# Optimization experiments

Measured on AMD Instinct MI355X. Metric: run time of the kernel, lower is better.

The kernel has to match this reference:

```python
import jax, jax.numpy as jnp
import numpy as np

H = 8            # n_heads
CAP = 512        # capacity
TOPK = 2
N_HOPS = 2
ROPE_BASE = 10000.0
VOCAB = 32000
D = 512


def rope_cos_sin(T, dh, base):
    inv = 1.0 / (base ** (jnp.arange(0, dh, 2, dtype=jnp.float32) / dh))
    f = jnp.arange(T, dtype=jnp.float32)[:, None] * inv[None, :]   # [T, dh/2]
    emb = jnp.concatenate([f, f], axis=-1)                          # [T, dh]
    return jnp.cos(emb), jnp.sin(emb)


def rmsnorm(x, s):
    return x * jax.lax.rsqrt(jnp.mean(x * x, axis=-1, keepdims=True) + 1e-6) * s


def rotate_half(x):
    x1, x2 = jnp.split(x, 2, axis=-1)
    return jnp.concatenate([-x2, x1], axis=-1)


def attn_block(x, cos, sin, wqkv, wo, ln_s):
    # pre-norm causal attention with RoPE; residual included (module returns x + attn)
    C, d = x.shape
    dh = d // H
    u = rmsnorm(x, ln_s)
    qkv = u @ wqkv.T                                   # [C, 3d]
    q, k, v = [t.reshape(C, H, dh) for t in jnp.split(qkv, 3, axis=-1)]
    c = cos[:, None, :]; s = sin[:, None, :]
    q = q * c + rotate_half(q) * s
    k = k * c + rotate_half(k) * s
    scores = jnp.einsum('qhd,khd->hqk', q, k) / jnp.sqrt(jnp.float32(dh))
    causal = jnp.tril(jnp.ones((C, C), dtype=bool))
    scores = jnp.where(causal[None], scores, -1e9)
    a = jax.nn.softmax(scores, axis=-1)
    o = jnp.einsum('hqk,khd->qhd', a, v).reshape(C, d)
    return x + o @ wo.T


def ffn_block(x, w1, w2, ln_s):
    u = rmsnorm(x, ln_s)
    return x + jax.nn.gelu(u @ w1.T) @ w2.T


def hop(h, wr, attn_qkv, attn_o, attn_ln, ffn_w1, ffn_w2, ffn_ln, cos, sin):
    T, d = h.shape
    E_total = wr.shape[0]
    E = E_total - 1                                    # last expert = identity
    logits = h @ wr.T                                  # [T, E_total]
    probs = jax.nn.softmax(logits, axis=-1)
    _, idx = jax.lax.top_k(logits, TOPK)
    mask = jax.nn.one_hot(idx, E_total).sum(axis=-2) > 0     # [T, E_total]
    probs_tr = probs[:, :-1]
    mask_tr = mask[:, :-1]
    # capacity select: per-expert top-cap gated tokens -> one-hot slot [E, cap, T]
    g = jnp.where(mask_tr.T, probs_tr.T, -jnp.inf)     # [E, T]
    cap = min(CAP, T)
    _, top_idx = jax.lax.top_k(g, cap)                 # [E, cap]
    slot = jnp.zeros((E, cap, T), jnp.float32).at[
        jnp.arange(E)[:, None], jnp.arange(cap)[None, :], top_idx].set(1.0)
    slot = slot * mask_tr.T[:, None, :]
    kept = slot.sum(axis=1) > 0                        # [E, T]
    # dispatch
    xin = jnp.einsum('ect,td->ecd', slot, h)
    cos_r = jnp.einsum('ect,td->ecd', slot, cos)
    sin_r = jnp.einsum('ect,td->ecd', slot, sin)
    attn_idx = jnp.arange(0, E, 2)
    ffn_idx = jnp.arange(1, E, 2)
    out_a = jax.vmap(attn_block)(xin[attn_idx], cos_r[attn_idx], sin_r[attn_idx],
                                 attn_qkv, attn_o, attn_ln)
    out_f = jax.vmap(ffn_block)(xin[ffn_idx], ffn_w1, ffn_w2, ffn_ln)
    expert_out = jnp.zeros_like(xin).at[attn_idx].set(out_a).at[ffn_idx].set(out_f)
    # combine
    combine_w = jnp.where(kept.T, probs_tr, 0.0)       # [T, E]
    rho = combine_w.sum(axis=-1, keepdims=True)        # [T, 1]
    combine = jnp.einsum('ecd,ect,et->td', expert_out, slot, combine_w.T)
    return h + combine - rho * h


def setup_inputs() -> dict:
    key = jax.random.key(0)
    ks = jax.random.split(key, 12)
    T = 2048
    sc = 0.02
    return {
        'ids': jax.random.randint(ks[0], (T,), 0, VOCAB),
        'embed_w': jax.random.normal(ks[1], (VOCAB, D), jnp.float32) * sc,
        'router_w': jax.random.normal(ks[2], (N_HOPS, 9, D), jnp.float32) * sc,
        'attn_qkv': jax.random.normal(ks[3], (4, 3 * D, D), jnp.float32) * sc,
        'attn_o': jax.random.normal(ks[4], (4, D, D), jnp.float32) * sc,
        'attn_ln': jnp.ones((4, D), jnp.float32),
        'ffn_w1': jax.random.normal(ks[5], (4, 4 * D, D), jnp.float32) * sc,
        'ffn_w2': jax.random.normal(ks[6], (4, D, 4 * D), jnp.float32) * sc,
        'ffn_ln': jnp.ones((4, D), jnp.float32),
        'bb_qkv': jax.random.normal(ks[7], (3 * D, D), jnp.float32) * sc,
        'bb_o': jax.random.normal(ks[8], (D, D), jnp.float32) * sc,
        'bb_ln': jnp.ones((D,), jnp.float32),
        'lnout_s': jnp.ones((D,), jnp.float32),
    }


def reference(ids, embed_w, router_w, attn_qkv, attn_o, attn_ln,
              ffn_w1, ffn_w2, ffn_ln, bb_qkv, bb_o, bb_ln, lnout_s):
    T = ids.shape[0]
    dh = D // H
    h = embed_w[ids]                                   # [T, D]
    cos, sin = rope_cos_sin(T, dh, ROPE_BASE)
    h = attn_block(h, cos, sin, bb_qkv, bb_o, bb_ln)   # backbone (num_backbone=1)
    for i in range(router_w.shape[0]):                 # n_hops routed layers
        h = hop(h, router_w[i], attn_qkv, attn_o, attn_ln,
                ffn_w1, ffn_w2, ffn_ln, cos, sin)
    return rmsnorm(h, lnout_s)
```

## Files before the change

### kernel.cpp

```cpp
#include <hip/hip_runtime.h>
#include <hip/hip_bf16.h>

#define T_SEQ 2048
#define DMODEL 512
#define CEXP 512

typedef short s16x4 __attribute__((ext_vector_type(4)));
typedef short s16x8 __attribute__((ext_vector_type(8)));
typedef float f32x4 __attribute__((ext_vector_type(4)));

__device__ __forceinline__ float geluf(float x){
  float x3 = x*x*x;
  return 0.5f*x*(1.f + tanhf(0.7978845608028654f*(x + 0.044715f*x3)));
}

__device__ __forceinline__ unsigned short f2b(float x){
  unsigned int u = __float_as_uint(x);
  u += 0x7fffu + ((u >> 16) & 1u);
  return (unsigned short)(u >> 16);
}

struct GP {
  const float* A; long As;
  const float* W; long Ws;
  const float* R; long Rs;
  float* O; long Os;
  int M, N, K, act;
};

__global__ void embed_kernel(const int* __restrict__ ids, const float* __restrict__ ew,
                             float* __restrict__ h){
  int idx = blockIdx.x*256 + threadIdx.x;
  int t = idx >> 9, d = idx & 511;
  h[idx] = ew[(size_t)ids[t]*DMODEL + d];
}

__global__ void rope_table_kernel(float* __restrict__ cosb, float* __restrict__ sinb){
  int idx = blockIdx.x*256 + threadIdx.x;
  int t = idx >> 6, i = idx & 63, j = i & 31;
  float inv = powf(10000.f, -(float)(2*j)/64.f);
  float a = (float)t * inv;
  cosb[idx] = cosf(a);
  sinb[idx] = sinf(a);
}

__global__ void rmsnorm_kernel(const float* __restrict__ in, float* __restrict__ out,
                               const float* __restrict__ scale,
                               int rows_per_group, long gstride, int scale_stride){
  int row = blockIdx.x;
  int g = row / rows_per_group, lr = row - g*rows_per_group;
  const float* x = in  + (size_t)g*gstride + (size_t)lr*DMODEL;
  float*       y = out + (size_t)g*gstride + (size_t)lr*DMODEL;
  const float* s = scale + (size_t)g*scale_stride;
  int tid = threadIdx.x;
  float ss = 0.f;
  for (int i = tid; i < DMODEL; i += 256){ float v = x[i]; ss += v*v; }
  __shared__ float red[256];
  red[tid] = ss; __syncthreads();
  for (int st = 128; st > 0; st >>= 1){ if (tid < st) red[tid] += red[tid+st]; __syncthreads(); }
  float r = rsqrtf(red[0]*(1.f/DMODEL) + 1e-6f);
  for (int i = tid; i < DMODEL; i += 256) y[i] = x[i]*r*s[i];
}

__global__ void final_rmsnorm_kernel(const float* __restrict__ in, float* __restrict__ out,
                                     const float* __restrict__ scale){
  int row = blockIdx.x;
  const float* x = in + (size_t)row*DMODEL;
  int tid = threadIdx.x;
  float ss = 0.f;
  for (int i = tid; i < DMODEL; i += 256){ float v = x[i]; ss += v*v; }
  __shared__ float red[256];
  red[tid] = ss; __syncthreads();
  for (int st = 128; st > 0; st >>= 1){ if (tid < st) red[tid] += red[tid+st]; __syncthreads(); }
  float r = rsqrtf(red[0]*(1.f/DMODEL) + 1e-6f);
  for (int i = tid; i < DMODEL; i += 256)
    out[(size_t)row*DMODEL + i] = x[i]*r*scale[i];
}

__device__ __forceinline__ void gemm64_body(GP g, int bx, int by, int bz){
  const float* A = g.A + (size_t)bz*g.As;
  const float* W = g.W + (size_t)bz*g.Ws;
  const float* Res = g.R ? g.R + (size_t)bz*g.Rs : nullptr;
  float* Out = g.O + (size_t)bz*g.Os;
  int M = g.M, N = g.N, K = g.K, act = g.act;
  __shared__ float As[16][68];
  __shared__ float Ws[16][68];
  int tid = threadIdx.x;
  int tx = tid & 15, ty = tid >> 4;
  int row0 = bx*64, col0 = by*64;
  float acc[4][4] = {{0.f}};
  int sm = tid >> 2;
  int skq = (tid & 3) << 2;
  int gm = row0 + sm, gn = col0 + sm;

  float4 va = make_float4(0.f,0.f,0.f,0.f);
  float4 vw = make_float4(0.f,0.f,0.f,0.f);
  if (gm < M) va = *(const float4*)&A[(size_t)gm*K + skq];
  if (gn < N) vw = *(const float4*)&W[(size_t)gn*K + skq];

  for (int k0 = 0; k0 < K; k0 += 16){
    __syncthreads();
    As[skq+0][sm] = va.x; As[skq+1][sm] = va.y; As[skq+2][sm] = va.z; As[skq+3][sm] = va.w;
    Ws[skq+0][sm] = vw.x; Ws[skq+1][sm] = vw.y; Ws[skq+2][sm] = vw.z; Ws[skq+3][sm] = vw.w;
    __syncthreads();
    if (k0 + 16 < K){
      if (gm < M) va = *(const float4*)&A[(size_t)gm*K + k0 + 16 + skq];
      if (gn < N) vw = *(const float4*)&W[(size_t)gn*K + k0 + 16 + skq];
    }
    #pragma unroll
    for (int kk = 0; kk < 16; ++kk){
      float4 av = *(const float4*)&As[kk][ty*4];
      float4 wv = *(const float4*)&Ws[kk][tx*4];
      float a[4] = {av.x, av.y, av.z, av.w};
      float w[4] = {wv.x, wv.y, wv.z, wv.w};
      #pragma unroll
      for (int i = 0; i < 4; ++i)
        #pragma unroll
        for (int j = 0; j < 4; ++j)
          acc[i][j] += a[i]*w[j];
    }
  }
  #pragma unroll
  for (int i = 0; i < 4; ++i){
    int om = row0 + ty*4 + i;
    if (om >= M) continue;
    #pragma unroll
    for (int j = 0; j < 4; ++j){
      int on = col0 + tx*4 + j;
      if (on >= N) continue;
      float v = acc[i][j];
      if (act == 1) v = geluf(v);
      if (Res) v += Res[(size_t)om*N + on];
      Out[(size_t)om*N + on] = v;
    }
  }
}

__global__ __launch_bounds__(256)
void gemm_kernel(GP g){ gemm64_body(g, blockIdx.x, blockIdx.y, blockIdx.z); }

__global__ __launch_bounds__(256)
void gemm_dual(GP g1, GP g2, int ysplit){
  bool first = (int)blockIdx.y < ysplit;
  GP g = first ? g1 : g2;
  int by = first ? blockIdx.y : blockIdx.y - ysplit;
  gemm64_body(g, blockIdx.x, by, blockIdx.z);
}

__global__ __launch_bounds__(256)
void gemm128(const float* __restrict__ A, long Astride,
             const float* __restrict__ W, long Wstride,
             const float* __restrict__ Res, long Rstride,
             float* __restrict__ Out, long Ostride,
             int M, int N, int K, int act){
  int b = blockIdx.z;
  A += (size_t)b*Astride; W += (size_t)b*Wstride; Out += (size_t)b*Ostride;
  if (Res) Res += (size_t)b*Rstride;
  __shared__ float As[16][132];
  __shared__ float Ws[16][132];
  int tid = threadIdx.x;
  int r0 = (tid >> 4) * 8;
  int c0 = (tid & 15) * 8;
  int row0 = blockIdx.x*128, col0 = blockIdx.y*128;
  int sr = tid >> 1;
  int sc = (tid & 1) * 8;
  float acc[8][8] = {{0.f}};

  float4 a0 = *(const float4*)&A[(size_t)(row0+sr)*K + sc];
  float4 a1 = *(const float4*)&A[(size_t)(row0+sr)*K + sc + 4];
  float4 w0 = *(const float4*)&W[(size_t)(col0+sr)*K + sc];
  float4 w1 = *(const float4*)&W[(size_t)(col0+sr)*K + sc + 4];

  for (int k0 = 0; k0 < K; k0 += 16){
    __syncthreads();
    As[sc+0][sr]=a0.x; As[sc+1][sr]=a0.y; As[sc+2][sr]=a0.z; As[sc+3][sr]=a0.w;
    As[sc+4][sr]=a1.x; As[sc+5][sr]=a1.y; As[sc+6][sr]=a1.z; As[sc+7][sr]=a1.w;
    Ws[sc+0][sr]=w0.x; Ws[sc+1][sr]=w0.y; Ws[sc+2][sr]=w0.z; Ws[sc+3][sr]=w0.w;
    Ws[sc+4][sr]=w1.x; Ws[sc+5][sr]=w1.y; Ws[sc+6][sr]=w1.z; Ws[sc+7][sr]=w1.w;
    __syncthreads();
    if (k0 + 16 < K){
      a0 = *(const float4*)&A[(size_t)(row0+sr)*K + k0 + 16 + sc];
      a1 = *(const float4*)&A[(size_t)(row0+sr)*K + k0 + 16 + sc + 4];
      w0 = *(const float4*)&W[(size_t)(col0+sr)*K + k0 + 16 + sc];
      w1 = *(const float4*)&W[(size_t)(col0+sr)*K + k0 + 16 + sc + 4];
    }
    #pragma unroll
    for (int kk = 0; kk < 16; ++kk){
      float a[8], w[8];
      *(float4*)&a[0] = *(const float4*)&As[kk][r0];
      *(float4*)&a[4] = *(const float4*)&As[kk][r0+4];
      *(float4*)&w[0] = *(const float4*)&Ws[kk][c0];
      *(float4*)&w[4] = *(const float4*)&Ws[kk][c0+4];
      #pragma unroll
      for (int i = 0; i < 8; ++i)
        #pragma unroll
        for (int j = 0; j < 8; ++j)
          acc[i][j] += a[i]*w[j];
    }
  }

  #pragma unroll
  for (int i = 0; i < 8; ++i){
    int gm = row0 + r0 + i;
    #pragma unroll
    for (int jj = 0; jj < 2; ++jj){
      int gn = col0 + c0 + jj*4;
      float4 v;
      v.x = acc[i][jj*4+0]; v.y = acc[i][jj*4+1];
      v.z = acc[i][jj*4+2]; v.w = acc[i][jj*4+3];
      if (act == 1){ v.x = geluf(v.x); v.y = geluf(v.y); v.z = geluf(v.z); v.w = geluf(v.w); }
      if (Res){
        float4 rv = *(const float4*)&Res[(size_t)gm*N + gn];
        v.x += rv.x; v.y += rv.y; v.z += rv.z; v.w += rv.w;
      }
      *(float4*)&Out[(size_t)gm*N + gn] = v;
    }
  }
}

__device__ __forceinline__ void mfma_body(GP g, int bx, int by, int bz){
  const float* A = g.A + (size_t)bz*g.As;
  const float* W = g.W + (size_t)bz*g.Ws;
  const float* Res = g.R ? g.R + (size_t)bz*g.Rs : nullptr;
  float* Out = g.O + (size_t)bz*g.Os;
  int N = g.N, K = g.K, act = g.act;

  __shared__ short As[128][40];
  __shared__ short Ws[128][40];

  int tid = threadIdx.x;
  int l = tid & 63, w = tid >> 6;
  int wrow = (w >> 1)*64, wcol = (w & 1)*64;
  int row0 = bx*128, col0 = by*128;
  int lm = l & 15, lq = l >> 4;

  f32x4 acc[4][4];
  #pragma unroll
  for (int i = 0; i < 4; ++i)
    #pragma unroll
    for (int j = 0; j < 4; ++j)
      acc[i][j] = (f32x4){0.f,0.f,0.f,0.f};

  for (int k0 = 0; k0 < K; k0 += 32){
    #pragma unroll
    for (int t = 0; t < 4; ++t){
      int f4 = tid + t*256;
      int r = f4 >> 3, kq = f4 & 7;
      float4 va = *(const float4*)&A[(size_t)(row0 + r)*K + k0 + kq*4];
      s16x4 pa; pa[0]=(short)f2b(va.x); pa[1]=(short)f2b(va.y); pa[2]=(short)f2b(va.z); pa[3]=(short)f2b(va.w);
      *(s16x4*)&As[r][kq*4] = pa;
      float4 vw = *(const float4*)&W[(size_t)(col0 + r)*K + k0 + kq*4];
      s16x4 pw; pw[0]=(short)f2b(vw.x); pw[1]=(short)f2b(vw.y); pw[2]=(short)f2b(vw.z); pw[3]=(short)f2b(vw.w);
      *(s16x4*)&Ws[r][kq*4] = pw;
    }
    __syncthreads();

    s16x8 af[4], bf[4];
    #pragma unroll
    for (int rt = 0; rt < 4; ++rt)
      af[rt] = *(s16x8*)&As[wrow + rt*16 + lm][lq*8];
    #pragma unroll
    for (int ct = 0; ct < 4; ++ct)
      bf[ct] = *(s16x8*)&Ws[wcol + ct*16 + lm][lq*8];
    #pragma unroll
    for (int rt = 0; rt < 4; ++rt)
      #pragma unroll
      for (int ct = 0; ct < 4; ++ct)
        acc[rt][ct] = __builtin_amdgcn_mfma_f32_16x16x32_bf16(af[rt], bf[ct], acc[rt][ct], 0, 0, 0);
    __syncthreads();
  }

  #pragma unroll
  for (int rt = 0; rt < 4; ++rt){
    #pragma unroll
    for (int p = 0; p < 4; ++p){
      int row = row0 + wrow + rt*16 + lq*4 + p;
      #pragma unroll
      for (int ct = 0; ct < 4; ++ct){
        int col = col0 + wcol + ct*16 + lm;
        float v = acc[rt][ct][p];
        if (act == 1) v = geluf(v);
        if (Res) v += Res[(size_t)row*N + col];
        Out[(size_t)row*N + col] = v;
      }
    }
  }
}

__global__ __launch_bounds__(256)
void gemm_mfma(GP g){ mfma_body(g, blockIdx.x, blockIdx.y, blockIdx.z); }

__global__ __launch_bounds__(256)
void mfma_dual(GP g1, GP g2, int ysplit){
  bool first = (int)blockIdx.y < ysplit;
  GP g = first ? g1 : g2;
  int by = first ? blockIdx.y : blockIdx.y - ysplit;
  mfma_body(g, blockIdx.x, by, blockIdx.z);
}

__global__ void rope_kernel(float* __restrict__ qkv, const float* __restrict__ cosb,
                            const float* __restrict__ sinb, const int* __restrict__ map,
                            int map_gstride, int rows_per_group){
  int idx = blockIdx.x*256 + threadIdx.x;
  int row = idx >> 9;
  int rem = idx & 511;
  int sec = rem >> 8;
  int hh  = (rem >> 5) & 7;
  int j   = rem & 31;
  int t;
  if (map){
    t = map[(row/rows_per_group)*map_gstride + (row % rows_per_group)];
    if (t < 0) return;
  } else {
    t = row;
  }
  float c = cosb[t*64 + j], s = sinb[t*64 + j];
  float* p = qkv + (size_t)row*1536 + sec*512 + hh*64;
  float a = p[j], b = p[j+32];
  p[j]    = a*c - b*s;
  p[j+32] = b*c + a*s;
}

__global__ __launch_bounds__(256, 3)
void fattn_kernel(const float* __restrict__ qkv, float* __restrict__ ctx, int C){
  int tps = C >> 4;
  int pairs = tps >> 1;
  int lin = blockIdx.y * gridDim.x + blockIdx.x;
  int hh  = lin & 7;
  int bx  = lin >> 3;
  int seq = bx / pairs;
  int pr  = bx - seq*pairs;
  size_t base = (size_t)seq * C * 1536;
  const float* Qg = qkv + base + hh*64;
  const float* Kg = qkv + base + 512 + hh*64;
  const float* Vg = qkv + base + 1024 + hh*64;

  __shared__ float Qs[16][68];
  __shared__ float Ks[64][68];
  __shared__ float Ps[16][68];

  int tid = threadIdx.x;
  int tx = tid & 15, ty = tid >> 4;

  #pragma unroll 1
  for (int half = 0; half < 2; ++half){
    int lt = half ? pr : (tps - 1 - pr);
    int q0 = lt << 4;
    if (half) __syncthreads();

    *(float4*)&Qs[ty][tx*4] = *(const float4*)&Qg[(size_t)(q0 + ty)*1536 + tx*4];

    float o[4] = {0.f, 0.f, 0.f, 0.f};
    float mrow = -1e30f, lrow = 0.f;

    int nkt = (lt >> 2) + 1;
    for (int kt = 0; kt < nkt; ++kt){
      int k0 = kt << 6;
      if (kt) __syncthreads();
      for (int i = tid; i < 64*16; i += 256){
        int r = i >> 4, dq = i & 15;
        *(float4*)&Ks[r][dq*4] = *(const float4*)&Kg[(size_t)(k0 + r)*1536 + dq*4];
      }
      __syncthreads();

      const float* vbase = Vg + (size_t)k0*1536 + tx*4;
      float4 nv0 = *(const float4*)(vbase + 0*1536);
      float4 nv1 = *(const float4*)(vbase + 1*1536);
      float4 nv2 = *(const float4*)(vbase + 2*1536);
      float4 nv3 = *(const float4*)(vbase + 3*1536);

      float s[4] = {0.f, 0.f, 0.f, 0.f};
      #pragma unroll
      for (int d = 0; d < 64; d += 4){
        float4 qv = *(const float4*)&Qs[ty][d];
        float4 kv[4];
        #pragma unroll
        for (int j = 0; j < 4; ++j) kv[j] = *(const float4*)&Ks[j*16+tx][d];
        #pragma unroll
        for (int j = 0; j < 4; ++j)
          s[j] += qv.x*kv[j].x + qv.y*kv[j].y + qv.z*kv[j].z + qv.w*kv[j].w;
      }
      {
        int q = q0 + ty;
        #pragma unroll
        for (int j = 0; j < 4; ++j){
          int k = k0 + j*16 + tx;
          s[j] = (k <= q) ? s[j]*0.125f : -1e30f;
        }
      }
      {
        float m2 = fmaxf(fmaxf(s[0], s[1]), fmaxf(s[2], s[3]));
        #pragma unroll
        for (int off = 1; off < 16; off <<= 1)
          m2 = fmaxf(m2, __shfl_xor(m2, off, 64));
        float mnew = fmaxf(mrow, m2);
        float alpha = __expf(mrow - mnew);
        float p0 = __expf(s[0] - mnew);
        float p1 = __expf(s[1] - mnew);
        float p2 = __expf(s[2] - mnew);
        float p3 = __expf(s[3] - mnew);
        float rs = (p0 + p1) + (p2 + p3);
        #pragma unroll
        for (int off = 1; off < 16; off <<= 1)
          rs += __shfl_xor(rs, off, 64);
        lrow = lrow*alpha + rs;
        mrow = mnew;
        #pragma unroll
        for (int j = 0; j < 4; ++j) o[j] *= alpha;
        Ps[ty][tx]    = p0;
        Ps[ty][16+tx] = p1;
        Ps[ty][32+tx] = p2;
        Ps[ty][48+tx] = p3;
      }
      {
        #pragma unroll
        for (int kc = 0; kc < 16; ++kc){
          float4 v0 = nv0, v1 = nv1, v2 = nv2, v3 = nv3;
          if (kc < 15){
            const float* nb = vbase + (size_t)(kc+1)*4*1536;
            nv0 = *(const float4*)(nb + 0*1536);
            nv1 = *(const float4*)(nb + 1*1536);
            nv2 = *(const float4*)(nb + 2*1536);
            nv3 = *(const float4*)(nb + 3*1536);
          }
          float4 pr4 = *(const float4*)&Ps[ty][kc*4];
          o[0] += pr4.x*v0.x + pr4.y*v1.x + pr4.z*v2.x + pr4.w*v3.x;
          o[1] += pr4.x*v0.y + pr4.y*v1.y + pr4.z*v2.y + pr4.w*v3.y;
          o[2] += pr4.x*v0.z + pr4.y*v1.z + pr4.z*v2.z + pr4.w*v3.z;
          o[3] += pr4.x*v0.w + pr4.y*v1.w + pr4.z*v2.w + pr4.w*v3.w;
        }
      }
    }

    float inv = 1.f / lrow;
    float4 res;
    res.x = o[0]*inv; res.y = o[1]*inv; res.z = o[2]*inv; res.w = o[3]*inv;
    *(float4*)(ctx + (size_t)(seq*C + q0 + ty)*512 + hh*64 + tx*4) = res;
  }
}

__global__ void router_kernel(const float* __restrict__ logits, float* __restrict__ probs,
                              int* __restrict__ maskb){
  int t = blockIdx.x*256 + threadIdx.x;
  if (t >= T_SEQ) return;
  float v[9];
  float mx = -1e30f;
  for (int e = 0; e < 9; ++e){ v[e] = logits[t*9+e]; mx = fmaxf(mx, v[e]); }
  float s = 0.f;
  for (int e = 0; e < 9; ++e) s += expf(v[e]-mx);
  float inv = 1.f/s;
  for (int e = 0; e < 8; ++e) probs[t*8+e] = expf(v[e]-mx)*inv;
  int i1 = 0;
  for (int e = 1; e < 9; ++e) if (v[e] > v[i1]) i1 = e;
  int i2 = -1;
  for (int e = 0; e < 9; ++e){ if (e == i1) continue; if (i2 < 0 || v[e] > v[i2]) i2 = e; }
  maskb[t] = (1<<i1) | (1<<i2);
}

__global__ void seti_kernel(int* __restrict__ p, int v, int n){
  int i = blockIdx.x*256 + threadIdx.x;
  if (i < n) p[i] = v;
}

__global__ void rank_kernel(const float* __restrict__ probs, const int* __restrict__ maskb,
                            int* __restrict__ t2s, int* __restrict__ s2t, float* __restrict__ cw){
  int idx = blockIdx.x*256 + threadIdx.x;
  int e = idx / T_SEQ, t = idx - e*T_SEQ;
  __shared__ float spm[T_SEQ];
  int tid = threadIdx.x;
  for (int i = tid; i < T_SEQ; i += 256)
    spm[i] = ((maskb[i]>>e)&1) ? probs[i*8+e] : -1.0f;
  __syncthreads();
  int slot = -1; float w = 0.f;
  if ((maskb[t]>>e)&1){
    float p = probs[t*8+e];
    int rank = 0;
    #pragma unroll 8
    for (int t2 = 0; t2 < T_SEQ; ++t2){
      float p2 = spm[t2];
      rank += (p2 > p || (p2 == p && t2 < t)) ? 1 : 0;
    }
    if (rank < CEXP){ slot = rank; w = p; s2t[e*CEXP + rank] = t; }
  }
  t2s[t*8+e] = slot;
  cw[t*8+e] = w;
}

__global__ void gather_kernel(const float* __restrict__ h, const int* __restrict__ s2t,
                              float* __restrict__ xin){
  int idx = blockIdx.x*256 + threadIdx.x;
  int row = idx >> 9, d = idx & 511;
  int t = s2t[row];
  xin[idx] = (t >= 0) ? h[(size_t)t*DMODEL + d] : 0.f;
}

__global__ void combine_kernel(float* __restrict__ h, const float* __restrict__ eout,
                               const int* __restrict__ t2s, const float* __restrict__ cw){
  int idx = blockIdx.x*256 + threadIdx.x;
  int t = idx >> 9, d = idx & 511;
  float acc = 0.f, rho = 0.f;
  for (int e = 0; e < 8; ++e){
    int c = t2s[t*8+e];
    if (c >= 0){
      float w = cw[t*8+e];
      rho += w;
      acc += w * eout[((size_t)e*CEXP + c)*DMODEL + d];
    }
  }
  float hv = h[idx];
  h[idx] = hv + acc - rho*hv;
}

extern "C" void kernel_launch(void* const* d_in, const int* in_sizes, int n_in,
                              void* d_out, int out_size, void* d_ws, size_t ws_size,
                              hipStream_t stream){
  const int*   ids      = (const int*)  d_in[0];
  const float* embed_w  = (const float*)d_in[1];
  const float* router_w = (const float*)d_in[2];
  const float* attn_qkv = (const float*)d_in[3];
  const float* attn_o   = (const float*)d_in[4];
  const float* attn_ln  = (const float*)d_in[5];
  const float* ffn_w1   = (const float*)d_in[6];
  const float* ffn_w2   = (const float*)d_in[7];
  const float* ffn_ln   = (const float*)d_in[8];
  const float* bb_qkv   = (const float*)d_in[9];
  const float* bb_o     = (const float*)d_in[10];
  const float* bb_ln    = (const float*)d_in[11];
  const float* lnout_s  = (const float*)d_in[12];
  float* out = (float*)d_out;

  float* W    = (float*)d_ws;
  float* h    = W;
  float* cosb = h    + 1048576;
  float* sinb = cosb + 131072;
  float* xin  = sinb + 131072;
  float* u    = xin  + 2097152;
  float* big  = u    + 2097152;
  float* ctx  = big  + 4194304;
  float* eout = ctx  + 1048576;
  float* logits = eout + 2097152;
  float* probs  = logits + 18432;
  float* cw     = probs  + 16384;
  int* ibase = (int*)(cw + 16384);
  int* maskb = ibase;
  int* t2s   = maskb + 2048;
  int* s2t   = t2s   + 16384;

  embed_kernel<<<4096, 256, 0, stream>>>(ids, embed_w, h);
  rope_table_kernel<<<512, 256, 0, stream>>>(cosb, sinb);

  rmsnorm_kernel<<<2048, 256, 0, stream>>>(h, u, bb_ln, 2048, 0, 0);
  gemm128<<<dim3(16,12,1), 256, 0, stream>>>(u, 0, bb_qkv, 0, nullptr, 0, big, 0,
                                             2048, 1536, 512, 0);
  rope_kernel<<<4096, 256, 0, stream>>>(big, cosb, sinb, nullptr, 0, 2048);
  fattn_kernel<<<dim3(64,8,1), 256, 0, stream>>>(big, ctx, 2048);
  gemm_kernel<<<dim3(32,8,1), 256, 0, stream>>>(
      GP{ctx, 0, bb_o, 0, h, 0, h, 0, 2048, 512, 512, 0});

  for (int hop = 0; hop < 2; ++hop){
    const float* wr = router_w + (size_t)hop*9*512;
    gemm_kernel<<<dim3(32,1,1), 256, 0, stream>>>(
        GP{h, 0, wr, 0, nullptr, 0, logits, 0, 2048, 9, 512, 0});
    router_kernel<<<8, 256, 0, stream>>>(logits, probs, maskb);
    seti_kernel<<<16, 256, 0, stream>>>(s2t, -1, 4096);
    rank_kernel<<<64, 256, 0, stream>>>(probs, maskb, t2s, s2t, cw);
    gather_kernel<<<8192, 256, 0, stream>>>(h, s2t, xin);

    rmsnorm_kernel<<<2048, 256, 0, stream>>>(xin,          u,          attn_ln, 512, 524288, 512);
    rmsnorm_kernel<<<2048, 256, 0, stream>>>(xin + 262144, u + 262144, ffn_ln,  512, 524288, 512);

    if (hop == 0){
      gemm128<<<dim3(4,12,4), 256, 0, stream>>>(u, 524288, attn_qkv, 786432, nullptr, 0,
                                                big, 786432, 512, 1536, 512, 0);
      rope_kernel<<<4096, 256, 0, stream>>>(big, cosb, sinb, s2t, 1024, 512);
      fattn_kernel<<<dim3(64,8,1), 256, 0, stream>>>(big, ctx, 512);
      gemm128<<<dim3(4,16,4), 256, 0, stream>>>(u + 262144, 524288, ffn_w1, 1048576,
                                                nullptr, 0, big, 1048576,
                                                512, 2048, 512, 1);
      gemm_dual<<<dim3(8,16,4), 256, 0, stream>>>(
          GP{ctx, 262144, attn_o, 262144, xin, 524288, eout, 524288, 512, 512, 512, 0},
          GP{big, 1048576, ffn_w2, 1048576, xin + 262144, 524288, eout + 262144, 524288, 512, 512, 2048, 0},
          8);
    } else {
      gemm_mfma<<<dim3(4,12,4), 256, 0, stream>>>(
          GP{u, 524288, attn_qkv, 786432, nullptr, 0, big, 786432, 512, 1536, 512, 0});
      rope_kernel<<<4096, 256, 0, stream>>>(big, cosb, sinb, s2t, 1024, 512);
      fattn_kernel<<<dim3(64,8,1), 256, 0, stream>>>(big, ctx, 512);
      gemm_mfma<<<dim3(4,16,4), 256, 0, stream>>>(
          GP{u + 262144, 524288, ffn_w1, 1048576, nullptr, 0, big, 1048576, 512, 2048, 512, 1});
      mfma_dual<<<dim3(4,8,4), 256, 0, stream>>>(
          GP{ctx, 262144, attn_o, 262144, xin, 524288, eout, 524288, 512, 512, 512, 0},
          GP{big, 1048576, ffn_w2, 1048576, xin + 262144, 524288, eout + 262144, 524288, 512, 512, 2048, 0},
          4);
    }

    combine_kernel<<<4096, 256, 0, stream>>>(h, eout, t2s, cw);
  }

  final_rmsnorm_kernel<<<2048, 256, 0, stream>>>(h, out, lnout_s);
}
```

Baseline: 1.234 ms.

## Vectorize elementwise kernels, fuse dual rmsnorm, stage 128 K rows per attention sync

Embed, gather and combine now move data as float4, so each launch uses a quarter as many threads and fewer, wider memory instructions. The two per-hop rmsnorm launches become one dual kernel that picks its input by block index, removing a launch. The flash-attention kernel loads 128 K rows into shared memory per barrier instead of 64 and processes them as two 64-row sub-tiles, halving the K-load barriers. The larger K buffer raises shared memory per block, which may reduce occupancy under the 3-blocks-per-CU launch bound.

```diff
diff --git a/kernel.cpp b/kernel.cpp
--- a/kernel.cpp
+++ b/kernel.cpp
@@ -31,8 +31,8 @@
 __global__ void embed_kernel(const int* __restrict__ ids, const float* __restrict__ ew,
                              float* __restrict__ h){
   int idx = blockIdx.x*256 + threadIdx.x;
-  int t = idx >> 9, d = idx & 511;
-  h[idx] = ew[(size_t)ids[t]*DMODEL + d];
+  int t = idx >> 7, d4 = idx & 127;
+  *(float4*)&h[(size_t)idx*4] = *(const float4*)&ew[(size_t)ids[t]*DMODEL + d4*4];
 }
 
 __global__ void rope_table_kernel(float* __restrict__ cosb, float* __restrict__ sinb){
@@ -48,6 +48,29 @@
                                const float* __restrict__ scale,
                                int rows_per_group, long gstride, int scale_stride){
   int row = blockIdx.x;
+  int g = row / rows_per_group, lr = row - g*rows_per_group;
+  const float* x = in  + (size_t)g*gstride + (size_t)lr*DMODEL;
+  float*       y = out + (size_t)g*gstride + (size_t)lr*DMODEL;
+  const float* s = scale + (size_t)g*scale_stride;
+  int tid = threadIdx.x;
+  float ss = 0.f;
+  for (int i = tid; i < DMODEL; i += 256){ float v = x[i]; ss += v*v; }
+  __shared__ float red[256];
+  red[tid] = ss; __syncthreads();
+  for (int st = 128; st > 0; st >>= 1){ if (tid < st) red[tid] += red[tid+st]; __syncthreads(); }
+  float r = rsqrtf(red[0]*(1.f/DMODEL) + 1e-6f);
+  for (int i = tid; i < DMODEL; i += 256) y[i] = x[i]*r*s[i];
+}
+
+__global__ void rmsnorm_dual_kernel(const float* __restrict__ in1, float* __restrict__ out1,
+                                    const float* __restrict__ sc1,
+                                    const float* __restrict__ in2, float* __restrict__ out2,
+                                    const float* __restrict__ sc2,
+                                    int rows_per_group, long gstride, int scale_stride, int nrows){
+  int row = blockIdx.x;
+  const float* in; float* out; const float* scale;
+  if (row < nrows){ in = in1; out = out1; scale = sc1; }
+  else            { in = in2; out = out2; scale = sc2; row -= nrows; }
   int g = row / rows_per_group, lr = row - g*rows_per_group;
   const float* x = in  + (size_t)g*gstride + (size_t)lr*DMODEL;
   float*       y = out + (size_t)g*gstride + (size_t)lr*DMODEL;
@@ -336,7 +359,7 @@
   const float* Vg = qkv + base + 1024 + hh*64;
 
   __shared__ float Qs[16][68];
-  __shared__ float Ks[64][68];
+  __shared__ float Ks[128][68];
   __shared__ float Ps[16][68];
 
   int tid = threadIdx.x;
@@ -354,80 +377,91 @@
     float mrow = -1e30f, lrow = 0.f;
 
     int nkt = (lt >> 2) + 1;
-    for (int kt = 0; kt < nkt; ++kt){
-      int k0 = kt << 6;
-      if (kt) __syncthreads();
-      for (int i = tid; i < 64*16; i += 256){
+    int nks = (nkt + 1) >> 1;
+    #pragma unroll 1
+    for (int ks = 0; ks < nks; ++ks){
+      int kbase = ks << 7;
+      int rows = (nkt << 6) - kbase; if (rows > 128) rows = 128;
+      if (ks) __syncthreads();
+      for (int i = tid; i < rows*16; i += 256){
         int r = i >> 4, dq = i & 15;
-        *(float4*)&Ks[r][dq*4] = *(const float4*)&Kg[(size_t)(k0 + r)*1536 + dq*4];
+        *(float4*)&Ks[r][dq*4] = *(const float4*)&Kg[(size_t)(kbase + r)*1536 + dq*4];
       }
       __syncthreads();
 
-      const float* vbase = Vg + (size_t)k0*1536 + tx*4;
-      float4 nv0 = *(const float4*)(vbase + 0*1536);
-      float4 nv1 = *(const float4*)(vbase + 1*1536);
-      float4 nv2 = *(const float4*)(vbase + 2*1536);
-      float4 nv3 = *(const float4*)(vbase + 3*1536);
-
-      float s[4] = {0.f, 0.f, 0.f, 0.f};
-      #pragma unroll
-      for (int d = 0; d < 64; d += 4){
-        float4 qv = *(const float4*)&Qs[ty][d];
-        float4 kv[4];
+      #pragma unroll 1
+      for (int sub = 0; sub < 2; ++sub){
+        int kt = (ks << 1) + sub;
+        if (kt >= nkt) break;
+        int k0 = kt << 6;
+        int kro = sub << 6;
+
+        const float* vbase = Vg + (size_t)k0*1536 + tx*4;
+        float4 nv0 = *(const float4*)(vbase + 0*1536);
+        float4 nv1 = *(const float4*)(vbase + 1*1536);
+        float4 nv2 = *(const float4*)(vbase + 2*1536);
+        float4 nv3 = *(const float4*)(vbase + 3*1536);
+
+        float s[4] = {0.f, 0.f, 0.f, 0.f};
         #pragma unroll
-        for (int j = 0; j < 4; ++j) kv[j] = *(const float4*)&Ks[j*16+tx][d];
-        #pragma unroll
-        for (int j = 0; j < 4; ++j)
-          s[j] += qv.x*kv[j].x + qv.y*kv[j].y + qv.z*kv[j].z + qv.w*kv[j].w;
-      }
-      {
-        int q = q0 + ty;
-        #pragma unroll
-        for (int j = 0; j < 4; ++j){
-          int k = k0 + j*16 + tx;
-          s[j] = (k <= q) ? s[j]*0.125f : -1e30f;
+        for (int d = 0; d < 64; d += 4){
+          float4 qv = *(const float4*)&Qs[ty][d];
+          float4 kv[4];
+          #pragma unroll
+          for (int j = 0; j < 4; ++j) kv[j] = *(const float4*)&Ks[kro + j*16+tx][d];
+          #pragma unroll
+          for (int j = 0; j < 4; ++j)
+            s[j] += qv.x*kv[j].x + qv.y*kv[j].y + qv.z*kv[j].z + qv.w*kv[j].w;
         }
-      }
-      {
-        float m2 = fmaxf(fmaxf(s[0], s[1]), fmaxf(s[2], s[3]));
-        #pragma unroll
-        for (int off = 1; off < 16; off <<= 1)
-          m2 = fmaxf(m2, __shfl_xor(m2, off, 64));
-        float mnew = fmaxf(mrow, m2);
-        float alpha = __expf(mrow - mnew);
-        float p0 = __expf(s[0] - mnew);
-        float p1 = __expf(s[1] - mnew);
-        float p2 = __expf(s[2] - mnew);
-        float p3 = __expf(s[3] - mnew);
-        float rs = (p0 + p1) + (p2 + p3);
-        #pragma unroll
-        for (int off = 1; off < 16; off <<= 1)
-          rs += __shfl_xor(rs, off, 64);
-        lrow = lrow*alpha + rs;
-        mrow = mnew;
-        #pragma unroll
-        for (int j = 0; j < 4; ++j) o[j] *= alpha;
-        Ps[ty][tx]    = p0;
-        Ps[ty][16+tx] = p1;
-        Ps[ty][32+tx] = p2;
-        Ps[ty][48+tx] = p3;
-      }
-      {
-        #pragma unroll
-        for (int kc = 0; kc < 16; ++kc){
-          float4 v0 = nv0, v1 = nv1, v2 = nv2, v3 = nv3;
-          if (kc < 15){
-            const float* nb = vbase + (size_t)(kc+1)*4*1536;
-            nv0 = *(const float4*)(nb + 0*1536);
-            nv1 = *(const float4*)(nb + 1*1536);
-            nv2 = *(const float4*)(nb + 2*1536);
-            nv3 = *(const float4*)(nb + 3*1536);
+        {
+          int q = q0 + ty;
+          #pragma unroll
+          for (int j = 0; j < 4; ++j){
+            int k = k0 + j*16 + tx;
+            s[j] = (k <= q) ? s[j]*0.125f : -1e30f;
           }
-          float4 pr4 = *(const float4*)&Ps[ty][kc*4];
-          o[0] += pr4.x*v0.x + pr4.y*v1.x + pr4.z*v2.x + pr4.w*v3.x;
-          o[1] += pr4.x*v0.y + pr4.y*v1.y + pr4.z*v2.y + pr4.w*v3.y;
-          o[2] += pr4.x*v0.z + pr4.y*v1.z + pr4.z*v2.z + pr4.w*v3.z;
-          o[3] += pr4.x*v0.w + pr4.y*v1.w + pr4.z*v2.w + pr4.w*v3.w;
+        }
+        {
+          float m2 = fmaxf(fmaxf(s[0], s[1]), fmaxf(s[2], s[3]));
+          #pragma unroll
+          for (int off = 1; off < 16; off <<= 1)
+            m2 = fmaxf(m2, __shfl_xor(m2, off, 64));
+          float mnew = fmaxf(mrow, m2);
+          float alpha = __expf(mrow - mnew);
+          float p0 = __expf(s[0] - mnew);
+          float p1 = __expf(s[1] - mnew);
+          float p2 = __expf(s[2] - mnew);
+          float p3 = __expf(s[3] - mnew);
+          float rs = (p0 + p1) + (p2 + p3);
+          #pragma unroll
+          for (int off = 1; off < 16; off <<= 1)
+            rs += __shfl_xor(rs, off, 64);
+          lrow = lrow*alpha + rs;
+          mrow = mnew;
+          #pragma unroll
+          for (int j = 0; j < 4; ++j) o[j] *= alpha;
+          Ps[ty][tx]    = p0;
+          Ps[ty][16+tx] = p1;
+          Ps[ty][32+tx] = p2;
+          Ps[ty][48+tx] = p3;
+        }
+        {
+          #pragma unroll
+          for (int kc = 0; kc < 16; ++kc){
+            float4 v0 = nv0, v1 = nv1, v2 = nv2, v3 = nv3;
+            if (kc < 15){
+              const float* nb = vbase + (size_t)(kc+1)*4*1536;
+              nv0 = *(const float4*)(nb + 0*1536);
+              nv1 = *(const float4*)(nb + 1*1536);
+              nv2 = *(const float4*)(nb + 2*1536);
+              nv3 = *(const float4*)(nb + 3*1536);
+            }
+            float4 pr4 = *(const float4*)&Ps[ty][kc*4];
+            o[0] += pr4.x*v0.x + pr4.y*v1.x + pr4.z*v2.x + pr4.w*v3.x;
+            o[1] += pr4.x*v0.y + pr4.y*v1.y + pr4.z*v2.y + pr4.w*v3.y;
+            o[2] += pr4.x*v0.z + pr4.y*v1.z + pr4.z*v2.z + pr4.w*v3.z;
+            o[3] += pr4.x*v0.w + pr4.y*v1.w + pr4.z*v2.w + pr4.w*v3.w;
+          }
         }
       }
     }
@@ -489,26 +523,35 @@
 __global__ void gather_kernel(const float* __restrict__ h, const int* __restrict__ s2t,
                               float* __restrict__ xin){
   int idx = blockIdx.x*256 + threadIdx.x;
-  int row = idx >> 9, d = idx & 511;
+  int row = idx >> 7, d4 = idx & 127;
   int t = s2t[row];
-  xin[idx] = (t >= 0) ? h[(size_t)t*DMODEL + d] : 0.f;
+  float4 v = make_float4(0.f,0.f,0.f,0.f);
+  if (t >= 0) v = *(const float4*)&h[(size_t)t*DMODEL + d4*4];
+  *(float4*)&xin[(size_t)idx*4] = v;
 }
 
 __global__ void combine_kernel(float* __restrict__ h, const float* __restrict__ eout,
                                const int* __restrict__ t2s, const float* __restrict__ cw){
   int idx = blockIdx.x*256 + threadIdx.x;
-  int t = idx >> 9, d = idx & 511;
-  float acc = 0.f, rho = 0.f;
+  int t = idx >> 7, d4 = idx & 127;
+  float4 acc = make_float4(0.f,0.f,0.f,0.f);
+  float rho = 0.f;
   for (int e = 0; e < 8; ++e){
     int c = t2s[t*8+e];
     if (c >= 0){
       float w = cw[t*8+e];
       rho += w;
-      acc += w * eout[((size_t)e*CEXP + c)*DMODEL + d];
-    }
-  }
-  float hv = h[idx];
-  h[idx] = hv + acc - rho*hv;
+      float4 ev = *(const float4*)&eout[((size_t)e*CEXP + c)*DMODEL + d4*4];
+      acc.x += w*ev.x; acc.y += w*ev.y; acc.z += w*ev.z; acc.w += w*ev.w;
+    }
+  }
+  float4 hv = *(float4*)&h[(size_t)idx*4];
+  float4 r;
+  r.x = hv.x + acc.x - rho*hv.x;
+  r.y = hv.y + acc.y - rho*hv.y;
+  r.z = hv.z + acc.z - rho*hv.z;
+  r.w = hv.w + acc.w - rho*hv.w;
+  *(float4*)&h[(size_t)idx*4] = r;
 }
 
 extern "C" void kernel_launch(void* const* d_in, const int* in_sizes, int n_in,
@@ -546,7 +589,7 @@
   int* t2s   = maskb + 2048;
   int* s2t   = t2s   + 16384;
 
-  embed_kernel<<<4096, 256, 0, stream>>>(ids, embed_w, h);
+  embed_kernel<<<1024, 256, 0, stream>>>(ids, embed_w, h);
   rope_table_kernel<<<512, 256, 0, stream>>>(cosb, sinb);
 
   rmsnorm_kernel<<<2048, 256, 0, stream>>>(h, u, bb_ln, 2048, 0, 0);
@@ -564,10 +607,11 @@
     router_kernel<<<8, 256, 0, stream>>>(logits, probs, maskb);
     seti_kernel<<<16, 256, 0, stream>>>(s2t, -1, 4096);
     rank_kernel<<<64, 256, 0, stream>>>(probs, maskb, t2s, s2t, cw);
-    gather_kernel<<<8192, 256, 0, stream>>>(h, s2t, xin);
-
-    rmsnorm_kernel<<<2048, 256, 0, stream>>>(xin,          u,          attn_ln, 512, 524288, 512);
-    rmsnorm_kernel<<<2048, 256, 0, stream>>>(xin + 262144, u + 262144, ffn_ln,  512, 524288, 512);
+    gather_kernel<<<2048, 256, 0, stream>>>(h, s2t, xin);
+
+    rmsnorm_dual_kernel<<<4096, 256, 0, stream>>>(xin,          u,          attn_ln,
+                                                  xin + 262144, u + 262144, ffn_ln,
+                                                  512, 524288, 512, 2048);
 
     if (hop == 0){
       gemm128<<<dim3(4,12,4), 256, 0, stream>>>(u, 524288, attn_qkv, 786432, nullptr, 0,
@@ -594,7 +638,7 @@
           4);
     }
 
-    combine_kernel<<<4096, 256, 0, stream>>>(h, eout, t2s, cw);
+    combine_kernel<<<1024, 256, 0, stream>>>(h, eout, t2s, cw);
   }
 
   final_rmsnorm_kernel<<<2048, 256, 0, stream>>>(h, out, lnout_s);
```

After: 1.439 ms. 1.17x slower.
